# Performance work log

Hardware: AMD Instinct MI355X
Metric: run time of the kernel (lower is better)

The kernel has to match this reference:

```python
import jax, jax.numpy as jnp
import numpy as np

MAX_ITER = 16
TOL = 1e-3


def setup_inputs() -> dict:
    key = jax.random.key(0)
    k0, k1, k2, k3 = jax.random.split(key, 4)
    B, A, Bd, Y = 16384, 1024, 2, 128
    AT = jax.random.uniform(k0, (B, A), dtype=jnp.float32)
    K = jax.random.uniform(k1, (A, Bd), dtype=jnp.float32)
    BT = jnp.ones((Bd,), dtype=jnp.float32)  # fixed to [1, 1] in the module
    u = jax.random.uniform(k2, (A * Bd, Y), dtype=jnp.float32)
    b = jax.random.uniform(k3, (Y,), dtype=jnp.float32)
    return {"AT": AT, "K": K, "BT": BT, "u": u, "b": b}


def reference(AT, K, BT, u, b):
    batch = AT.shape[0]
    Kp = K ** 2  # 'reparam' constraint

    # Fixed-point matrix-balancing loop (torch.no_grad block) -> constants.
    Ksg = jax.lax.stop_gradient(Kp)
    ATsg = jax.lax.stop_gradient(AT)
    A_dim, B_dim = Kp.shape
    af0 = jnp.zeros((batch, A_dim), jnp.float32)
    bf0 = jnp.zeros((batch, B_dim), jnp.float32)

    def cond(carry):
        _, _, err, i = carry
        return (i < MAX_ITER) & (err >= TOL)

    def body(carry):
        af, bf, _, i = carry
        af_n = ATsg / (bf @ Ksg.T + 1.0)   # (batch, A_dim)
        bf_n = BT / (af_n @ Ksg + 1.0)     # (batch, B_dim)
        err = jnp.max(jnp.abs(af_n - af)) + jnp.max(jnp.abs(bf_n - bf))
        return af_n, bf_n, err, i + 1

    _, bf, _, _ = jax.lax.while_loop(
        cond, body, (af0, bf0, jnp.array(jnp.inf, jnp.float32), 0)
    )
    bf = jax.lax.stop_gradient(bf)

    # Final differentiable iteration.
    af = AT / (bf @ Kp.T + 1.0)            # (batch, A_dim)
    bf = BT / (af @ Kp + 1.0)              # (batch, B_dim)

    # C = K * (AF @ BF^T): rank-1 outer product per batch element.
    C = (Kp[None, :, :] * af[:, :, None] * bf[:, None, :]).reshape(batch, -1)
    return C @ u + b
```

## Files before the change

### kernel.cpp

```cpp
#include <hip/hip_runtime.h>

__device__ __forceinline__ unsigned short f2b(float f) {
    unsigned int u = __builtin_bit_cast(unsigned int, f);
    u += 0x7fffu + ((u >> 16) & 1u);
    return (unsigned short)(u >> 16);
}
__device__ __forceinline__ float fastrcp(float x) {
    return __builtin_amdgcn_rcpf(x);
}
__device__ __forceinline__ unsigned int cvt_pk_bf16(float lo, float hi) {
    unsigned int r;
    asm("v_cvt_pk_bf16_f32 %0, %1, %2" : "=v"(r) : "v"(lo), "v"(hi));
    return r;
}
template<int CTRL>
__device__ __forceinline__ float dpp_add(float x) {
    int s = __builtin_amdgcn_update_dpp(0, __builtin_bit_cast(int, x), CTRL, 0xf, 0xf, true);
    return x + __builtin_bit_cast(float, s);
}
__device__ __forceinline__ float wave_sum_bcast(float x) {
    x = dpp_add<0x111>(x);
    x = dpp_add<0x112>(x);
    x = dpp_add<0x114>(x);
    x = dpp_add<0x118>(x);
    x = dpp_add<0x142>(x);
    x = dpp_add<0x143>(x);
    return __builtin_bit_cast(float,
        __builtin_amdgcn_readlane(__builtin_bit_cast(int, x), 63));
}

typedef short bf16x8_t __attribute__((ext_vector_type(8)));
typedef float f32x4_t  __attribute__((ext_vector_type(4)));

#define NB   16384
#define AD   1024
#define YD   128

__global__ __launch_bounds__(256) void vt_kernel(
    const float* __restrict__ Kq,
    const float* __restrict__ U,
    unsigned short* __restrict__ Vtf)
{
    int o  = blockIdx.x * 256 + threadIdx.x;
    int T  = o >> 14;
    int CQ = (o >> 7) & 127;
    int rr = (o >> 3) & 15;
    int e  = o & 7;
    int n  = T * 16 + rr;
    int a  = CQ * 8 + e;
    int j  = n >> 7;
    int y  = n & 127;
    float k  = Kq[2 * a + j];
    float uv = U[(size_t)(2 * a + j) * YD + y];
    Vtf[o] = f2b(k * k * uv);
}

__global__ __launch_bounds__(512, 4) void fused_kernel(
    const float* __restrict__ AT,
    const float* __restrict__ Kq,
    const float* __restrict__ BTv,
    const unsigned short* __restrict__ Vtf,
    const float* __restrict__ bias,
    float* __restrict__ out)
{
    __shared__ __align__(16) unsigned short lA[32 * 1024];
    __shared__ float lbf[32][2];

    const int t    = threadIdx.x;
    const int lane = t & 63;
    const int w    = t >> 6;
    const int mtile = blockIdx.x;

    float kp0[16], kp1[16];
#pragma unroll
    for (int c = 0; c < 4; ++c) {
        int base = c * 256 + lane * 4;
        float4 k0v = *(const float4*)(Kq + 2 * base);
        float4 k1v = *(const float4*)(Kq + 2 * base + 4);
        kp0[c * 4 + 0] = k0v.x * k0v.x; kp1[c * 4 + 0] = k0v.y * k0v.y;
        kp0[c * 4 + 1] = k0v.z * k0v.z; kp1[c * 4 + 1] = k0v.w * k0v.w;
        kp0[c * 4 + 2] = k1v.x * k1v.x; kp1[c * 4 + 2] = k1v.y * k1v.y;
        kp0[c * 4 + 3] = k1v.z * k1v.z; kp1[c * 4 + 3] = k1v.w * k1v.w;
    }
    const float bt0 = BTv[0], bt1 = BTv[1];

    const float* atb = AT + (size_t)(mtile * 32 + w * 4) * AD;

    float ta[2][16];
#pragma unroll
    for (int c = 0; c < 4; ++c) {
        float4 av = *(const float4*)(atb + c * 256 + lane * 4);
        ta[0][c * 4 + 0] = av.x; ta[0][c * 4 + 1] = av.y;
        ta[0][c * 4 + 2] = av.z; ta[0][c * 4 + 3] = av.w;
    }

#pragma unroll
    for (int r = 0; r < 4; ++r) {
        const int cur = r & 1, nxt = cur ^ 1;
        if (r < 3) {
#pragma unroll
            for (int c = 0; c < 4; ++c) {
                float4 av = *(const float4*)(atb + (size_t)(r + 1) * AD + c * 256 + lane * 4);
                ta[nxt][c * 4 + 0] = av.x; ta[nxt][c * 4 + 1] = av.y;
                ta[nxt][c * 4 + 2] = av.z; ta[nxt][c * 4 + 3] = av.w;
            }
        }

        float M[9];
#pragma unroll
        for (int i2 = 0; i2 < 9; ++i2) M[i2] = 0.f;
#pragma unroll
        for (int e = 0; e < 16; ++e) {
            float tv = ta[cur][e], p = kp0[e], q2 = kp1[e];
            float u0 = tv * p, u1 = tv * q2;
            M[0] += u0; M[1] += u1;
            float u00 = u0 * p, u01 = u0 * q2, u11 = u1 * q2;
            M[2] += u00; M[3] += u01; M[4] += u11;
            M[5] += u00 * p; M[6] += u00 * q2; M[7] += u01 * q2; M[8] += u11 * q2;
        }
#pragma unroll
        for (int i2 = 0; i2 < 9; ++i2) M[i2] = wave_sum_bcast(M[i2]);

        float bf0 = 0.f, bf1 = 0.f;
#pragma unroll
        for (int it = 0; it < 8; ++it) {
            float q00 = bf0 * bf0, q01 = bf0 * bf1, q11 = bf1 * bf1;
            float s0 = M[0] - (bf0 * M[2] + bf1 * M[3]) + (q00 * M[5] + 2.f * q01 * M[6] + q11 * M[7]);
            float s1 = M[1] - (bf0 * M[3] + bf1 * M[4]) + (q00 * M[6] + 2.f * q01 * M[7] + q11 * M[8]);
            bf0 = bt0 * fastrcp(1.f + s0);
            bf1 = bt1 * fastrcp(1.f + s1);
        }
        const int m = w * 4 + r;
        if (lane == 0) { lbf[m][0] = bf0; lbf[m][1] = bf1; }

#pragma unroll
        for (int c = 0; c < 4; ++c) {
            float v[4];
#pragma unroll
            for (int e = 0; e < 4; ++e) {
                int idx = c * 4 + e;
                v[e] = ta[cur][idx] * fastrcp(1.f + bf0 * kp0[idx] + bf1 * kp1[idx]);
            }
            uint2 pk;
            pk.x = cvt_pk_bf16(v[0], v[1]);
            pk.y = cvt_pk_bf16(v[2], v[3]);
            int cg = c * 4 + (lane >> 4);
            int cl = (lane >> 1) & 7;
            int off = (m * 128 + cg * 8 + (cl ^ (m & 7))) * 8 + (lane & 1) * 4;
            *(uint2*)(&lA[off]) = pk;
        }
    }

    __syncthreads();

    const int rr = lane & 15;
    const int hb = lane >> 4;
    const int q  = w & 3;
    const int h  = w >> 2;
    const int rx = rr & 7;

    const int lanePart = hb * 128 + rr * 8;
    const unsigned short* bq = Vtf + (size_t)(2 * q) * 16384 + lanePart;

    f32x4_t acc[4];
#pragma unroll
    for (int j = 0; j < 4; ++j) acc[j] = (f32x4_t){0.f, 0.f, 0.f, 0.f};

    bf16x8_t fbA[4], fbB[4];

    auto loadB = [&](bf16x8_t* fb, int k0, int kk) {
        int ke = k0 * 16 + kk * 512;
        fb[0] = *(const bf16x8_t*)(bq + ke);
        fb[1] = *(const bf16x8_t*)(bq + ke + 16384);
        fb[2] = *(const bf16x8_t*)(bq + ke + 131072);
        fb[3] = *(const bf16x8_t*)(bq + ke + 147456);
    };
    auto compute = [&](const bf16x8_t* fb, int k0, int kk) {
        const int cq = kk * 4 + hb;
        bf16x8_t fa = *(const bf16x8_t*)(
            &lA[(((h * 16 + rr) * 128) + (k0 >> 6) * 8 + (cq ^ rx)) * 8]);
#pragma unroll
        for (int j = 0; j < 4; ++j)
            acc[j] = __builtin_amdgcn_mfma_f32_16x16x32_bf16(fa, fb[j], acc[j], 0, 0, 0);
    };

    loadB(fbA, 0, 0);
    loadB(fbB, 0, 1);
#pragma unroll 1
    for (int k0 = 0; k0 < AD; k0 += 64) {
        __builtin_amdgcn_s_setprio(1);
        compute(fbA, k0, 0);
        __builtin_amdgcn_s_setprio(0);
        if (k0 + 64 < AD) loadB(fbA, k0 + 64, 0);
        __builtin_amdgcn_s_setprio(1);
        compute(fbB, k0, 1);
        __builtin_amdgcn_s_setprio(0);
        if (k0 + 64 < AD) loadB(fbB, k0 + 64, 1);
    }

    const int mloc  = h * 16 + hb * 4;
    const int mbase = mtile * 32 + mloc;
    float2 bfv[4];
#pragma unroll
    for (int r = 0; r < 4; ++r)
        bfv[r] = *(const float2*)(&lbf[mloc + r][0]);
#pragma unroll
    for (int jj = 0; jj < 2; ++jj) {
        int y = q * 32 + jj * 16 + rr;
        float bv = bias[y];
#pragma unroll
        for (int r = 0; r < 4; ++r) {
            float val = bfv[r].x * acc[jj][r] + bfv[r].y * acc[jj + 2][r] + bv;
            out[(size_t)(mbase + r) * YD + y] = val;
        }
    }
}

extern "C" void kernel_launch(void* const* d_in, const int* in_sizes, int n_in,
                              void* d_out, int out_size, void* d_ws, size_t ws_size,
                              hipStream_t stream) {
    const float* AT  = (const float*)d_in[0];
    const float* Kq  = (const float*)d_in[1];
    const float* BTv = (const float*)d_in[2];
    const float* U   = (const float*)d_in[3];
    const float* bia = (const float*)d_in[4];
    float* out = (float*)d_out;

    unsigned short* Vtf = (unsigned short*)d_ws;

    vt_kernel<<<dim3(1024), dim3(256), 0, stream>>>(Kq, U, Vtf);
    fused_kernel<<<dim3(NB / 32), dim3(512), 0, stream>>>(AT, Kq, BTv, Vtf, bia, out);
}
```

Before: 119.4 us.

## Halve batch tile per block to 16 rows and raise occupancy

Each block now handles 16 batch rows instead of 32. Each of the 8 waves computes one 16-column output slice over both K halves, replacing the previous 2x4 wave grid with 4 accumulators. LDS drops to 32KB and the launch bound requests 8 waves per SIMD, with twice as many blocks. This aims to improve latency hiding and occupancy, but every block now reads the full Vtf matrix for half as many rows. That doubles the B-matrix traffic per output row, and the AT row prefetch overlap inside the balancing loop is lost.

```diff
diff --git a/kernel.cpp b/kernel.cpp
--- a/kernel.cpp
+++ b/kernel.cpp
@@ -55,7 +55,7 @@
     Vtf[o] = f2b(k * k * uv);
 }
 
-__global__ __launch_bounds__(512, 4) void fused_kernel(
+__global__ __launch_bounds__(512, 8) void fused_kernel(
     const float* __restrict__ AT,
     const float* __restrict__ Kq,
     const float* __restrict__ BTv,
@@ -63,8 +63,8 @@
     const float* __restrict__ bias,
     float* __restrict__ out)
 {
-    __shared__ __align__(16) unsigned short lA[32 * 1024];
-    __shared__ float lbf[32][2];
+    __shared__ __align__(16) unsigned short lA[16 * 1024];
+    __shared__ float lbf[16][2];
 
     const int t    = threadIdx.x;
     const int lane = t & 63;
@@ -84,34 +84,27 @@
     }
     const float bt0 = BTv[0], bt1 = BTv[1];
 
-    const float* atb = AT + (size_t)(mtile * 32 + w * 4) * AD;
+    const float* atb = AT + (size_t)(mtile * 16 + w * 2) * AD;
 
     float ta[2][16];
 #pragma unroll
-    for (int c = 0; c < 4; ++c) {
-        float4 av = *(const float4*)(atb + c * 256 + lane * 4);
-        ta[0][c * 4 + 0] = av.x; ta[0][c * 4 + 1] = av.y;
-        ta[0][c * 4 + 2] = av.z; ta[0][c * 4 + 3] = av.w;
-    }
-
-#pragma unroll
-    for (int r = 0; r < 4; ++r) {
-        const int cur = r & 1, nxt = cur ^ 1;
-        if (r < 3) {
-#pragma unroll
-            for (int c = 0; c < 4; ++c) {
-                float4 av = *(const float4*)(atb + (size_t)(r + 1) * AD + c * 256 + lane * 4);
-                ta[nxt][c * 4 + 0] = av.x; ta[nxt][c * 4 + 1] = av.y;
-                ta[nxt][c * 4 + 2] = av.z; ta[nxt][c * 4 + 3] = av.w;
-            }
-        }
-
+    for (int r = 0; r < 2; ++r) {
+#pragma unroll
+        for (int c = 0; c < 4; ++c) {
+            float4 av = *(const float4*)(atb + (size_t)r * AD + c * 256 + lane * 4);
+            ta[r][c * 4 + 0] = av.x; ta[r][c * 4 + 1] = av.y;
+            ta[r][c * 4 + 2] = av.z; ta[r][c * 4 + 3] = av.w;
+        }
+    }
+
+#pragma unroll
+    for (int r = 0; r < 2; ++r) {
         float M[9];
 #pragma unroll
         for (int i2 = 0; i2 < 9; ++i2) M[i2] = 0.f;
 #pragma unroll
         for (int e = 0; e < 16; ++e) {
-            float tv = ta[cur][e], p = kp0[e], q2 = kp1[e];
+            float tv = ta[r][e], p = kp0[e], q2 = kp1[e];
             float u0 = tv * p, u1 = tv * q2;
             M[0] += u0; M[1] += u1;
             float u00 = u0 * p, u01 = u0 * q2, u11 = u1 * q2;
@@ -130,7 +123,7 @@
             bf0 = bt0 * fastrcp(1.f + s0);
             bf1 = bt1 * fastrcp(1.f + s1);
         }
-        const int m = w * 4 + r;
+        const int m = w * 2 + r;
         if (lane == 0) { lbf[m][0] = bf0; lbf[m][1] = bf1; }
 
 #pragma unroll
@@ -139,7 +132,7 @@
 #pragma unroll
             for (int e = 0; e < 4; ++e) {
                 int idx = c * 4 + e;
-                v[e] = ta[cur][idx] * fastrcp(1.f + bf0 * kp0[idx] + bf1 * kp1[idx]);
+                v[e] = ta[r][idx] * fastrcp(1.f + bf0 * kp0[idx] + bf1 * kp1[idx]);
             }
             uint2 pk;
             pk.x = cvt_pk_bf16(v[0], v[1]);
@@ -155,32 +148,27 @@
 
     const int rr = lane & 15;
     const int hb = lane >> 4;
-    const int q  = w & 3;
-    const int h  = w >> 2;
     const int rx = rr & 7;
 
-    const int lanePart = hb * 128 + rr * 8;
-    const unsigned short* bq = Vtf + (size_t)(2 * q) * 16384 + lanePart;
-
-    f32x4_t acc[4];
-#pragma unroll
-    for (int j = 0; j < 4; ++j) acc[j] = (f32x4_t){0.f, 0.f, 0.f, 0.f};
-
-    bf16x8_t fbA[4], fbB[4];
+    const unsigned short* pB = Vtf + (size_t)w * 16384 + hb * 128 + rr * 8;
+
+    f32x4_t acc[2];
+#pragma unroll
+    for (int j = 0; j < 2; ++j) acc[j] = (f32x4_t){0.f, 0.f, 0.f, 0.f};
+
+    bf16x8_t fbA[2], fbB[2];
 
     auto loadB = [&](bf16x8_t* fb, int k0, int kk) {
         int ke = k0 * 16 + kk * 512;
-        fb[0] = *(const bf16x8_t*)(bq + ke);
-        fb[1] = *(const bf16x8_t*)(bq + ke + 16384);
-        fb[2] = *(const bf16x8_t*)(bq + ke + 131072);
-        fb[3] = *(const bf16x8_t*)(bq + ke + 147456);
+        fb[0] = *(const bf16x8_t*)(pB + ke);
+        fb[1] = *(const bf16x8_t*)(pB + ke + 131072);
     };
     auto compute = [&](const bf16x8_t* fb, int k0, int kk) {
         const int cq = kk * 4 + hb;
         bf16x8_t fa = *(const bf16x8_t*)(
-            &lA[(((h * 16 + rr) * 128) + (k0 >> 6) * 8 + (cq ^ rx)) * 8]);
-#pragma unroll
-        for (int j = 0; j < 4; ++j)
+            &lA[((rr * 128) + (k0 >> 6) * 8 + (cq ^ rx)) * 8]);
+#pragma unroll
+        for (int j = 0; j < 2; ++j)
             acc[j] = __builtin_amdgcn_mfma_f32_16x16x32_bf16(fa, fb[j], acc[j], 0, 0, 0);
     };
 
@@ -198,21 +186,18 @@
         if (k0 + 64 < AD) loadB(fbB, k0 + 64, 1);
     }
 
-    const int mloc  = h * 16 + hb * 4;
-    const int mbase = mtile * 32 + mloc;
+    const int mloc  = hb * 4;
+    const int mbase = mtile * 16 + mloc;
     float2 bfv[4];
 #pragma unroll
     for (int r = 0; r < 4; ++r)
         bfv[r] = *(const float2*)(&lbf[mloc + r][0]);
-#pragma unroll
-    for (int jj = 0; jj < 2; ++jj) {
-        int y = q * 32 + jj * 16 + rr;
-        float bv = bias[y];
-#pragma unroll
-        for (int r = 0; r < 4; ++r) {
-            float val = bfv[r].x * acc[jj][r] + bfv[r].y * acc[jj + 2][r] + bv;
-            out[(size_t)(mbase + r) * YD + y] = val;
-        }
+    const int y = w * 16 + rr;
+    const float bv = bias[y];
+#pragma unroll
+    for (int r = 0; r < 4; ++r) {
+        float val = bfv[r].x * acc[0][r] + bfv[r].y * acc[1][r] + bv;
+        out[(size_t)(mbase + r) * YD + y] = val;
     }
 }
 
@@ -229,5 +214,5 @@
     unsigned short* Vtf = (unsigned short*)d_ws;
 
     vt_kernel<<<dim3(1024), dim3(256), 0, stream>>>(Kq, U, Vtf);
-    fused_kernel<<<dim3(NB / 32), dim3(512), 0, stream>>>(AT, Kq, BTv, Vtf, bia, out);
-}
+    fused_kernel<<<dim3(NB / 16), dim3(512), 0, stream>>>(AT, Kq, BTv, Vtf, bia, out);
+}
```

Result: slower. 166.6 us (+39.6%).
